# Performance work log

Hardware: AMD Instinct MI355X
Metric: run time of the kernel (lower is better)

## Reference

```python
import jax, jax.numpy as jnp
import numpy as np

B, N, D, H = 4, 1024, 256, 8  # batch, seq, in_dim(=per-head qkv_dim), n_heads


def setup_inputs() -> dict:
    key = jax.random.key(0)
    k1, k2, k3 = jax.random.split(key, 3)
    x = jax.random.normal(k1, (B, N, D), dtype=jnp.float32)
    Wqkv = jax.random.normal(k2, (D, 3 * D * H), dtype=jnp.float32) * 0.02
    bqkv = jnp.zeros((3 * D * H,), dtype=jnp.float32)
    W0 = jax.random.normal(k3, (D * H, D), dtype=jnp.float32) * 0.02
    b0 = jnp.zeros((D,), dtype=jnp.float32)
    return {"x": x, "Wqkv": Wqkv, "bqkv": bqkv, "W0": W0, "b0": b0}


def reference(x, Wqkv, bqkv, W0, b0):
    b, n, d = x.shape
    h = Wqkv.shape[1] // (3 * d)
    qkv = x @ Wqkv + bqkv                      # [b, n, 3*d*h]
    # Faithful to torch: raw row-major reinterpretation of the buffer.
    q, k, v = jnp.reshape(qkv, (3, b, n, d, h))
    score = jnp.einsum('bnqh,btqh->bnth', q, k) * (d ** -0.5)  # [b, n, n, h]
    attn = jax.nn.softmax(score, axis=1)       # softmax over query axis (dim=1), as in source
    # einsum 'bnnh,bnqh->bnqh' = diagonal of attn times v (faithful to source)
    av = jnp.einsum('bnnh,bnqh->bnqh', attn, v)  # [b, n, d, h]
    out = av.reshape(b, n, d * h) @ W0 + b0    # [b, n, d]
    return out
```

## Files before the change

kernel.cpp:

```cpp
#include <hip/hip_runtime.h>


#define SEGSZ 8388608

typedef short v8s __attribute__((ext_vector_type(8)));
typedef float v4f __attribute__((ext_vector_type(4)));

__device__ __forceinline__ ushort f2bf(float v) {
  union { float f; unsigned u; } x; x.f = v;
  const unsigned r = x.u + 0x7fff + ((x.u >> 16) & 1);
  return (ushort)(r >> 16);
}
__device__ __forceinline__ float bf2f(ushort v) {
  union { unsigned u; float f; } x; x.u = ((unsigned)v) << 16;
  return x.f;
}

#define GLOAD_LDS16(g, l)                                            \
  __builtin_amdgcn_global_load_lds(                                  \
      (const __attribute__((address_space(1))) void*)(g),            \
      (__attribute__((address_space(3))) void*)(l), 16, 0, 0)

__global__ __launch_bounds__(256) void prep(
    const float* __restrict__ X, const float* __restrict__ Wqkv,
    const float* __restrict__ W0, ushort* __restrict__ xb,
    ushort* __restrict__ whT, ushort* __restrict__ w0T) {
  __shared__ float T[64][65];
  const int tid = threadIdx.x;
  int bid = blockIdx.x;

  if (bid < 1024) {
    const size_t i = ((size_t)bid * 256 + tid) * 4;
    const float4 v = *(const float4*)&X[i];
    ushort4 hv = {f2bf(v.x), f2bf(v.y), f2bf(v.z), f2bf(v.w)};
    *(ushort4*)&xb[i] = hv;
    return;
  }
  bid -= 1024;
  if (bid < 384) {
    const int n0 = (bid % 96) * 64;
    const int k0 = (bid / 96) * 64;
    {
      const int row = tid >> 2;
      const int c0 = (tid & 3) * 16;
#pragma unroll
      for (int j = 0; j < 16; j += 4) {
        const float4 v = *(const float4*)&Wqkv[(size_t)(k0 + row) * 6144 + n0 + c0 + j];
        T[row][c0 + j + 0] = v.x; T[row][c0 + j + 1] = v.y;
        T[row][c0 + j + 2] = v.z; T[row][c0 + j + 3] = v.w;
      }
    }
    __syncthreads();
    {
      const int nn = tid >> 2;
      const int kk0 = (tid & 3) * 16;
      const int n = n0 + nn;
      const int seg = n >> 11, h = n & 7, d = (n & 2047) >> 3;
      const int p = seg * 2048 + h * 256 + d;
      ushort hv[16];
#pragma unroll
      for (int j = 0; j < 16; ++j) hv[j] = f2bf(T[kk0 + j][nn]);
      const size_t base = (size_t)p * 256 + k0 + kk0;
#pragma unroll
      for (int j = 0; j < 16; j += 8) *(v8s*)&whT[base + j] = *(v8s*)&hv[j];
    }
    return;
  }
  bid -= 384;
  {
    const int e0 = (bid & 3) * 64;
    const int k0 = (bid >> 2) * 64;
    {
      const int row = tid >> 2;
      const int c0 = (tid & 3) * 16;
#pragma unroll
      for (int j = 0; j < 16; j += 4) {
        const float4 v = *(const float4*)&W0[(size_t)(k0 + row) * 256 + e0 + c0 + j];
        T[row][c0 + j + 0] = v.x; T[row][c0 + j + 1] = v.y;
        T[row][c0 + j + 2] = v.z; T[row][c0 + j + 3] = v.w;
      }
    }
    __syncthreads();
    {
      const int ee = tid >> 2;
      const int kk0 = (tid & 3) * 16;
#pragma unroll
      for (int j = 0; j < 16; ++j) {
        const int k = k0 + kk0 + j;
        const int d = k >> 3, h = k & 7;
        w0T[(size_t)(e0 + ee) * 2048 + h * 256 + d] = f2bf(T[kk0 + j][ee]);
      }
    }
  }
}

__global__ __launch_bounds__(256) void qkv_mfma(
    const ushort* __restrict__ xb, const ushort* __restrict__ whT,
    const float* __restrict__ bias, ushort* __restrict__ qkvb) {
  __shared__ ushort As[128 * 32];
  __shared__ ushort Bh[128 * 32];
  const int tid = threadIdx.x;
  const int wave = tid >> 6, lane = tid & 63;
  const int quad = lane >> 4, l15 = lane & 15;
  const int c0 = blockIdx.x * 128;
  const int r0 = blockIdx.y * 128;
  const int wr = (wave >> 1) * 64;
  const int wc = (wave & 1) * 64;

  v4f acc[4][4] = {};

  for (int d0 = 0; d0 < 256; d0 += 32) {
#pragma unroll
    for (int half = 0; half < 2; ++half) {
      const int rr = wave * 32 + half * 16;
      const int row = rr + (lane >> 2);
      const int gcol = d0 + (lane & 3) * 8;
      GLOAD_LDS16(xb + (size_t)(r0 + row) * 256 + gcol, &As[rr * 32]);
      GLOAD_LDS16(whT + (size_t)(c0 + row) * 256 + gcol, &Bh[rr * 32]);
    }
    __syncthreads();

    v8s aF[4], bF[4];
#pragma unroll
    for (int i = 0; i < 4; ++i) {
      aF[i] = *(const v8s*)&As[(wr + i * 16 + l15) * 32 + quad * 8];
      bF[i] = *(const v8s*)&Bh[(wc + i * 16 + l15) * 32 + quad * 8];
    }
#pragma unroll
    for (int ri = 0; ri < 4; ++ri)
#pragma unroll
      for (int ci = 0; ci < 4; ++ci)
        acc[ri][ci] = __builtin_amdgcn_mfma_f32_16x16x32_bf16(
            aF[ri], bF[ci], acc[ri][ci], 0, 0, 0);
    __syncthreads();
  }

#pragma unroll
  for (int ci = 0; ci < 4; ++ci) {
    const int c = c0 + wc + ci * 16 + l15;
    const int cseg = c >> 11;
    const int h = (c & 2047) >> 8;
    const int d = c & 255;
    const float bv = bias[cseg * 2048 + d * 8 + h];
#pragma unroll
    for (int ri = 0; ri < 4; ++ri)
#pragma unroll
      for (int rg = 0; rg < 4; ++rg) {
        const int r = r0 + wr + ri * 16 + quad * 4 + rg;
        const int g = r * 3 + cseg;
        const int seg = g >> 12;
        const int tok = g & 4095;
        float val = acc[ri][ci][rg] + bv;
        if (seg == 0) val *= 0.0625f;
        qkvb[(size_t)seg * SEGSZ + (size_t)tok * 2048 + h * 256 + d] = f2bf(val);
      }
  }
}

__global__ __launch_bounds__(256) void scores_mfma(
    const ushort* __restrict__ qkvb, float* __restrict__ pl,
    float* __restrict__ sd_ws) {
  __shared__ ushort Qs[128 * 32];
  __shared__ ushort Ks[128 * 32];
  __shared__ float redL[2][2][64];

  const int tid = threadIdx.x;
  const int wave = tid >> 6, lane = tid & 63;
  const int quad = lane >> 4, l15 = lane & 15;
  const int bh = blockIdx.z * 8 + blockIdx.x;
  const int tile = blockIdx.y;
  const int tt0 = (tile >> 3) * 128;
  const int nn0 = (tile & 7) * 128;
  const int b = bh >> 3, h = bh & 7;
  const ushort* Qg = qkvb + (size_t)b * 1024 * 2048 + h * 256;
  const ushort* Kg = Qg + SEGSZ;

  const int wr = (wave >> 1) * 64;
  const int wc = (wave & 1) * 64;

  v4f acc[4][4] = {};

  for (int d0 = 0; d0 < 256; d0 += 32) {
#pragma unroll
    for (int half = 0; half < 2; ++half) {
      const int rr = wave * 32 + half * 16;
      const int row = rr + (lane >> 2);
      const int gcol = d0 + (lane & 3) * 8;
      GLOAD_LDS16(Qg + (size_t)(nn0 + row) * 2048 + gcol, &Qs[rr * 32]);
      GLOAD_LDS16(Kg + (size_t)(tt0 + row) * 2048 + gcol, &Ks[rr * 32]);
    }
    __syncthreads();

    v8s aF[4], bF[4];
#pragma unroll
    for (int i = 0; i < 4; ++i) {
      aF[i] = *(const v8s*)&Qs[(wr + i * 16 + l15) * 32 + quad * 8];
      bF[i] = *(const v8s*)&Ks[(wc + i * 16 + l15) * 32 + quad * 8];
    }
#pragma unroll
    for (int ri = 0; ri < 4; ++ri)
#pragma unroll
      for (int ci = 0; ci < 4; ++ci)
        acc[ri][ci] =
            __builtin_amdgcn_mfma_f32_16x16x32_bf16(aF[ri], bF[ci], acc[ri][ci], 0, 0, 0);
    __syncthreads();
  }

  float lsum[4];
#pragma unroll
  for (int ci = 0; ci < 4; ++ci) {
    float s = 0.f;
#pragma unroll
    for (int ri = 0; ri < 4; ++ri)
#pragma unroll
      for (int rg = 0; rg < 4; ++rg) s += __expf(acc[ri][ci][rg]);
    s += __shfl_xor(s, 16, 64);
    s += __shfl_xor(s, 32, 64);
    lsum[ci] = s;
  }
  if (quad == 0) {
#pragma unroll
    for (int ci = 0; ci < 4; ++ci)
      redL[wave & 1][wave >> 1][ci * 16 + l15] = lsum[ci];
  }
  __syncthreads();
  if ((wave >> 1) == 0 && quad == 0) {
#pragma unroll
    for (int ci = 0; ci < 4; ++ci) {
      const int t = tt0 + (wave & 1) * 64 + ci * 16 + l15;
      const float l = lsum[ci] + redL[wave & 1][1][ci * 16 + l15];
      pl[((size_t)bh * 1024 + t) * 8 + (tile & 7)] = l;
    }
  }

  if (tt0 == nn0 && (wave == 0 || wave == 3) && quad == (l15 >> 2)) {
#pragma unroll
    for (int ri = 0; ri < 4; ++ri) {
      const int t = tt0 + (wave & 1) * 64 + ri * 16 + l15;
      sd_ws[(size_t)bh * 1024 + t] = acc[ri][ri][l15 & 3];
    }
  }
}

template <bool ATOMIC>
__global__ __launch_bounds__(256) void av_mfma(
    const ushort* __restrict__ vb, const ushort* __restrict__ w0T,
    const float* __restrict__ pl, const float* __restrict__ sd,
    ushort* __restrict__ partial, float* __restrict__ out) {
  __shared__ ushort As[128 * 32];
  __shared__ ushort Bs[128 * 32];
  __shared__ float diagS[128];
  const int tid = threadIdx.x;
  const int wave = tid >> 6, lane = tid & 63;
  const int quad = lane >> 4, l15 = lane & 15;
  const int e0 = blockIdx.x * 128;
  const int tok0 = blockIdx.y * 128;
  const int h = blockIdx.z;
  const int kbase = h * 256;
  const int wr = (wave >> 1) * 64;
  const int wc = (wave & 1) * 64;

  if (tid < 128) {
    const int bh = (tok0 >> 10) * 8 + h;
    const int t = (tok0 & 1023) + tid;
    const size_t base = ((size_t)bh * 1024 + t) * 8;
    float l = 0.f;
#pragma unroll
    for (int c = 0; c < 8; ++c) l += pl[base + c];
    diagS[tid] = __expf(sd[(size_t)bh * 1024 + t]) / l;
  }

  v4f acc[4][4] = {};

  for (int d0 = 0; d0 < 256; d0 += 32) {
#pragma unroll
    for (int half = 0; half < 2; ++half) {
      const int rr = wave * 32 + half * 16;
      const int row = rr + (lane >> 2);
      const int gcol = kbase + d0 + (lane & 3) * 8;
      GLOAD_LDS16(vb + (size_t)(tok0 + row) * 2048 + gcol, &As[rr * 32]);
      GLOAD_LDS16(w0T + (size_t)(e0 + row) * 2048 + gcol, &Bs[rr * 32]);
    }
    __syncthreads();

    v8s aF[4], bF[4];
#pragma unroll
    for (int i = 0; i < 4; ++i) {
      aF[i] = *(const v8s*)&As[(wr + i * 16 + l15) * 32 + quad * 8];
      bF[i] = *(const v8s*)&Bs[(wc + i * 16 + l15) * 32 + quad * 8];
    }
#pragma unroll
    for (int ri = 0; ri < 4; ++ri)
#pragma unroll
      for (int ci = 0; ci < 4; ++ci)
        acc[ri][ci] =
            __builtin_amdgcn_mfma_f32_16x16x32_bf16(aF[ri], bF[ci], acc[ri][ci], 0, 0, 0);
    __syncthreads();
  }

#pragma unroll
  for (int ri = 0; ri < 4; ++ri)
#pragma unroll
    for (int rg = 0; rg < 4; ++rg) {
      const int lrow = wr + ri * 16 + quad * 4 + rg;
      const int tok = tok0 + lrow;
      const float dg = diagS[lrow];
#pragma unroll
      for (int ci = 0; ci < 4; ++ci) {
        const int e = e0 + wc + ci * 16 + l15;
        const float val = acc[ri][ci][rg] * dg;
        if (ATOMIC)
          atomicAdd(&out[(size_t)tok * 256 + e], val);
        else
          partial[(size_t)h * 1048576 + (size_t)tok * 256 + e] = f2bf(val);
      }
    }
}

__global__ void init_out(const float* __restrict__ b0, float* __restrict__ out) {
  const int i = blockIdx.x * 256 + threadIdx.x;
  const int e0 = (i & 63) << 2;
  *(float4*)&out[(size_t)i * 4] = *(const float4*)&b0[e0];
}

__global__ void reduce_out(const ushort* __restrict__ partial,
                           const float* __restrict__ b0, float* __restrict__ out) {
  const int i = blockIdx.x * 256 + threadIdx.x;
  const int e0 = (i & 63) << 2;
  float4 a = *(const float4*)&b0[e0];
#pragma unroll
  for (int h = 0; h < 8; ++h) {
    const ushort4 p = *(const ushort4*)&partial[(size_t)h * 1048576 + (size_t)i * 4];
    a.x += bf2f(p.x); a.y += bf2f(p.y); a.z += bf2f(p.z); a.w += bf2f(p.w);
  }
  *(float4*)&out[(size_t)i * 4] = a;
}

extern "C" void kernel_launch(void* const* d_in, const int* in_sizes, int n_in,
                              void* d_out, int out_size, void* d_ws, size_t ws_size,
                              hipStream_t stream) {
  const float* x    = (const float*)d_in[0];
  const float* Wqkv = (const float*)d_in[1];
  const float* bqkv = (const float*)d_in[2];
  const float* W0   = (const float*)d_in[3];
  const float* b0   = (const float*)d_in[4];
  float* out = (float*)d_out;

  float*  pl   = (float*)d_ws;
  float*  sd   = pl + 262144;
  ushort* qkvb = (ushort*)(sd + 32768);
  ushort* xb   = qkvb + 3 * (size_t)SEGSZ;
  ushort* whT  = xb + 1048576;
  ushort* w0T  = whT + 1572864;
  ushort* partial = w0T + 524288;

  ushort* vb = qkvb + 2 * (size_t)SEGSZ;

  const size_t need_base =
      (size_t)(262144 + 32768) * 4 + (size_t)SEGSZ * 3 * 2 +
      (size_t)(1048576 + 1572864 + 524288) * 2;
  const bool full = ws_size >= need_base + (size_t)8 * 1048576 * 2;

  prep<<<1536, 256, 0, stream>>>(x, Wqkv, W0, xb, whT, w0T);
  qkv_mfma<<<dim3(48, 32), 256, 0, stream>>>(xb, whT, bqkv, qkvb);
  scores_mfma<<<dim3(8, 64, 4), 256, 0, stream>>>(qkvb, pl, sd);
  if (full) {
    av_mfma<false><<<dim3(2, 32, 8), 256, 0, stream>>>(vb, w0T, pl, sd, partial, out);
    reduce_out<<<1024, 256, 0, stream>>>(partial, b0, out);
  } else {
    init_out<<<1024, 256, 0, stream>>>(b0, out);
    av_mfma<true><<<dim3(2, 32, 8), 256, 0, stream>>>(vb, w0T, pl, sd, nullptr, out);
  }
}
```

Baseline: 141.4 us.

## Keep K strip resident in LDS for scores and widen QKV/AV block tiles

The scores kernel now loads a full 128x256 K strip into LDS once per block and loops over four 128-row Q tiles, accumulating column exp-sums across them. That cuts K reloads and the partial-sum array from 8 slots to 2 per token. The QKV and AV GEMMs move to 512-thread blocks with 256-wide tiles (256 rows in QKV, the full 256 output columns in AV), so shared operands are reused more and the grid is halved. In exchange, the scores kernel uses about 72KB of LDS, runs 4x fewer blocks, and has a long serial loop, which lowers occupancy and parallelism.

```diff
diff --git a/kernel.cpp b/kernel.cpp
--- a/kernel.cpp
+++ b/kernel.cpp
@@ -94,16 +94,16 @@
   }
 }
 
-__global__ __launch_bounds__(256) void qkv_mfma(
+__global__ __launch_bounds__(512) void qkv_mfma(
     const ushort* __restrict__ xb, const ushort* __restrict__ whT,
     const float* __restrict__ bias, ushort* __restrict__ qkvb) {
-  __shared__ ushort As[128 * 32];
+  __shared__ ushort As[256 * 32];
   __shared__ ushort Bh[128 * 32];
   const int tid = threadIdx.x;
   const int wave = tid >> 6, lane = tid & 63;
   const int quad = lane >> 4, l15 = lane & 15;
   const int c0 = blockIdx.x * 128;
-  const int r0 = blockIdx.y * 128;
+  const int r0 = blockIdx.y * 256;
   const int wr = (wave >> 1) * 64;
   const int wc = (wave & 1) * 64;
 
@@ -111,12 +111,15 @@
 
   for (int d0 = 0; d0 < 256; d0 += 32) {
 #pragma unroll
-    for (int half = 0; half < 2; ++half) {
-      const int rr = wave * 32 + half * 16;
-      const int row = rr + (lane >> 2);
-      const int gcol = d0 + (lane & 3) * 8;
-      GLOAD_LDS16(xb + (size_t)(r0 + row) * 256 + gcol, &As[rr * 32]);
-      GLOAD_LDS16(whT + (size_t)(c0 + row) * 256 + gcol, &Bh[rr * 32]);
+    for (int h2 = 0; h2 < 2; ++h2) {
+      const int rr = wave * 32 + h2 * 16;
+      const int row = rr + (lane >> 2);
+      GLOAD_LDS16(xb + (size_t)(r0 + row) * 256 + d0 + (lane & 3) * 8, &As[rr * 32]);
+    }
+    {
+      const int rr = wave * 16;
+      const int row = rr + (lane >> 2);
+      GLOAD_LDS16(whT + (size_t)(c0 + row) * 256 + d0 + (lane & 3) * 8, &Bh[rr * 32]);
     }
     __syncthreads();
 
@@ -160,17 +163,17 @@
 __global__ __launch_bounds__(256) void scores_mfma(
     const ushort* __restrict__ qkvb, float* __restrict__ pl,
     float* __restrict__ sd_ws) {
+  __shared__ ushort Ks[8 * 128 * 32];
   __shared__ ushort Qs[128 * 32];
-  __shared__ ushort Ks[128 * 32];
   __shared__ float redL[2][2][64];
 
   const int tid = threadIdx.x;
   const int wave = tid >> 6, lane = tid & 63;
   const int quad = lane >> 4, l15 = lane & 15;
   const int bh = blockIdx.z * 8 + blockIdx.x;
-  const int tile = blockIdx.y;
-  const int tt0 = (tile >> 3) * 128;
-  const int nn0 = (tile & 7) * 128;
+  const int strip = blockIdx.y;
+  const int tt0 = (strip >> 1) * 128;
+  const int half = strip & 1;
   const int b = bh >> 3, h = bh & 7;
   const ushort* Qg = qkvb + (size_t)b * 1024 * 2048 + h * 256;
   const ushort* Kg = Qg + SEGSZ;
@@ -178,108 +181,124 @@
   const int wr = (wave >> 1) * 64;
   const int wc = (wave & 1) * 64;
 
-  v4f acc[4][4] = {};
-
-  for (int d0 = 0; d0 < 256; d0 += 32) {
-#pragma unroll
-    for (int half = 0; half < 2; ++half) {
-      const int rr = wave * 32 + half * 16;
-      const int row = rr + (lane >> 2);
-      const int gcol = d0 + (lane & 3) * 8;
-      GLOAD_LDS16(Qg + (size_t)(nn0 + row) * 2048 + gcol, &Qs[rr * 32]);
-      GLOAD_LDS16(Kg + (size_t)(tt0 + row) * 2048 + gcol, &Ks[rr * 32]);
-    }
-    __syncthreads();
-
-    v8s aF[4], bF[4];
-#pragma unroll
-    for (int i = 0; i < 4; ++i) {
-      aF[i] = *(const v8s*)&Qs[(wr + i * 16 + l15) * 32 + quad * 8];
-      bF[i] = *(const v8s*)&Ks[(wc + i * 16 + l15) * 32 + quad * 8];
-    }
-#pragma unroll
-    for (int ri = 0; ri < 4; ++ri)
-#pragma unroll
-      for (int ci = 0; ci < 4; ++ci)
-        acc[ri][ci] =
-            __builtin_amdgcn_mfma_f32_16x16x32_bf16(aF[ri], bF[ci], acc[ri][ci], 0, 0, 0);
-    __syncthreads();
-  }
-
-  float lsum[4];
+#pragma unroll
+  for (int c = 0; c < 8; ++c)
+#pragma unroll
+    for (int h2 = 0; h2 < 2; ++h2) {
+      const int rr = wave * 32 + h2 * 16;
+      const int row = rr + (lane >> 2);
+      GLOAD_LDS16(Kg + (size_t)(tt0 + row) * 2048 + c * 32 + (lane & 3) * 8,
+                  &Ks[c * 4096 + rr * 32]);
+    }
+
+  float colsum[4] = {0.f, 0.f, 0.f, 0.f};
+
+  for (int i = 0; i < 4; ++i) {
+    const int nn0 = half * 512 + i * 128;
+    v4f acc[4][4] = {};
+#pragma unroll
+    for (int c = 0; c < 8; ++c) {
+#pragma unroll
+      for (int h2 = 0; h2 < 2; ++h2) {
+        const int rr = wave * 32 + h2 * 16;
+        const int row = rr + (lane >> 2);
+        GLOAD_LDS16(Qg + (size_t)(nn0 + row) * 2048 + c * 32 + (lane & 3) * 8,
+                    &Qs[rr * 32]);
+      }
+      __syncthreads();
+
+      v8s aF[4], bF[4];
+#pragma unroll
+      for (int j = 0; j < 4; ++j) {
+        aF[j] = *(const v8s*)&Qs[(wr + j * 16 + l15) * 32 + quad * 8];
+        bF[j] = *(const v8s*)&Ks[c * 4096 + (wc + j * 16 + l15) * 32 + quad * 8];
+      }
+#pragma unroll
+      for (int ri = 0; ri < 4; ++ri)
+#pragma unroll
+        for (int ci = 0; ci < 4; ++ci)
+          acc[ri][ci] = __builtin_amdgcn_mfma_f32_16x16x32_bf16(
+              aF[ri], bF[ci], acc[ri][ci], 0, 0, 0);
+      __syncthreads();
+    }
+#pragma unroll
+    for (int ci = 0; ci < 4; ++ci) {
+      float s = 0.f;
+#pragma unroll
+      for (int ri = 0; ri < 4; ++ri)
+#pragma unroll
+        for (int rg = 0; rg < 4; ++rg) s += __expf(acc[ri][ci][rg]);
+      colsum[ci] += s;
+    }
+    if (nn0 == tt0 && (wave == 0 || wave == 3) && quad == (l15 >> 2)) {
+#pragma unroll
+      for (int ri = 0; ri < 4; ++ri) {
+        const int t = tt0 + (wave & 1) * 64 + ri * 16 + l15;
+        sd_ws[(size_t)bh * 1024 + t] = acc[ri][ri][l15 & 3];
+      }
+    }
+  }
+
 #pragma unroll
   for (int ci = 0; ci < 4; ++ci) {
-    float s = 0.f;
-#pragma unroll
-    for (int ri = 0; ri < 4; ++ri)
-#pragma unroll
-      for (int rg = 0; rg < 4; ++rg) s += __expf(acc[ri][ci][rg]);
-    s += __shfl_xor(s, 16, 64);
-    s += __shfl_xor(s, 32, 64);
-    lsum[ci] = s;
+    colsum[ci] += __shfl_xor(colsum[ci], 16, 64);
+    colsum[ci] += __shfl_xor(colsum[ci], 32, 64);
   }
   if (quad == 0) {
 #pragma unroll
     for (int ci = 0; ci < 4; ++ci)
-      redL[wave & 1][wave >> 1][ci * 16 + l15] = lsum[ci];
+      redL[wave & 1][wave >> 1][ci * 16 + l15] = colsum[ci];
   }
   __syncthreads();
   if ((wave >> 1) == 0 && quad == 0) {
 #pragma unroll
     for (int ci = 0; ci < 4; ++ci) {
       const int t = tt0 + (wave & 1) * 64 + ci * 16 + l15;
-      const float l = lsum[ci] + redL[wave & 1][1][ci * 16 + l15];
-      pl[((size_t)bh * 1024 + t) * 8 + (tile & 7)] = l;
-    }
-  }
-
-  if (tt0 == nn0 && (wave == 0 || wave == 3) && quad == (l15 >> 2)) {
-#pragma unroll
-    for (int ri = 0; ri < 4; ++ri) {
-      const int t = tt0 + (wave & 1) * 64 + ri * 16 + l15;
-      sd_ws[(size_t)bh * 1024 + t] = acc[ri][ri][l15 & 3];
+      const float l = colsum[ci] + redL[wave & 1][1][ci * 16 + l15];
+      pl[((size_t)bh * 1024 + t) * 2 + half] = l;
     }
   }
 }
 
 template <bool ATOMIC>
-__global__ __launch_bounds__(256) void av_mfma(
+__global__ __launch_bounds__(512) void av_mfma(
     const ushort* __restrict__ vb, const ushort* __restrict__ w0T,
     const float* __restrict__ pl, const float* __restrict__ sd,
     ushort* __restrict__ partial, float* __restrict__ out) {
   __shared__ ushort As[128 * 32];
-  __shared__ ushort Bs[128 * 32];
+  __shared__ ushort Bs[256 * 32];
   __shared__ float diagS[128];
   const int tid = threadIdx.x;
   const int wave = tid >> 6, lane = tid & 63;
   const int quad = lane >> 4, l15 = lane & 15;
-  const int e0 = blockIdx.x * 128;
-  const int tok0 = blockIdx.y * 128;
-  const int h = blockIdx.z;
+  const int tok0 = blockIdx.x * 128;
+  const int h = blockIdx.y;
   const int kbase = h * 256;
-  const int wr = (wave >> 1) * 64;
-  const int wc = (wave & 1) * 64;
+  const int wr = (wave >> 2) * 64;
+  const int wc = (wave & 3) * 64;
 
   if (tid < 128) {
     const int bh = (tok0 >> 10) * 8 + h;
     const int t = (tok0 & 1023) + tid;
-    const size_t base = ((size_t)bh * 1024 + t) * 8;
-    float l = 0.f;
-#pragma unroll
-    for (int c = 0; c < 8; ++c) l += pl[base + c];
-    diagS[tid] = __expf(sd[(size_t)bh * 1024 + t]) / l;
+    const size_t base = ((size_t)bh * 1024 + t) * 2;
+    diagS[tid] = __expf(sd[(size_t)bh * 1024 + t]) / (pl[base] + pl[base + 1]);
   }
 
   v4f acc[4][4] = {};
 
   for (int d0 = 0; d0 < 256; d0 += 32) {
-#pragma unroll
-    for (int half = 0; half < 2; ++half) {
-      const int rr = wave * 32 + half * 16;
-      const int row = rr + (lane >> 2);
-      const int gcol = kbase + d0 + (lane & 3) * 8;
-      GLOAD_LDS16(vb + (size_t)(tok0 + row) * 2048 + gcol, &As[rr * 32]);
-      GLOAD_LDS16(w0T + (size_t)(e0 + row) * 2048 + gcol, &Bs[rr * 32]);
+    {
+      const int rr = wave * 16;
+      const int row = rr + (lane >> 2);
+      GLOAD_LDS16(vb + (size_t)(tok0 + row) * 2048 + kbase + d0 + (lane & 3) * 8,
+                  &As[rr * 32]);
+    }
+#pragma unroll
+    for (int h2 = 0; h2 < 2; ++h2) {
+      const int rr = wave * 32 + h2 * 16;
+      const int row = rr + (lane >> 2);
+      GLOAD_LDS16(w0T + (size_t)row * 2048 + kbase + d0 + (lane & 3) * 8,
+                  &Bs[rr * 32]);
     }
     __syncthreads();
 
@@ -307,7 +326,7 @@
       const float dg = diagS[lrow];
 #pragma unroll
       for (int ci = 0; ci < 4; ++ci) {
-        const int e = e0 + wc + ci * 16 + l15;
+        const int e = wc + ci * 16 + l15;
         const float val = acc[ri][ci][rg] * dg;
         if (ATOMIC)
           atomicAdd(&out[(size_t)tok * 256 + e], val);
@@ -347,7 +366,7 @@
   float* out = (float*)d_out;
 
   float*  pl   = (float*)d_ws;
-  float*  sd   = pl + 262144;
+  float*  sd   = pl + 65536;
   ushort* qkvb = (ushort*)(sd + 32768);
   ushort* xb   = qkvb + 3 * (size_t)SEGSZ;
   ushort* whT  = xb + 1048576;
@@ -357,18 +376,18 @@
   ushort* vb = qkvb + 2 * (size_t)SEGSZ;
 
   const size_t need_base =
-      (size_t)(262144 + 32768) * 4 + (size_t)SEGSZ * 3 * 2 +
+      (size_t)(65536 + 32768) * 4 + (size_t)SEGSZ * 3 * 2 +
       (size_t)(1048576 + 1572864 + 524288) * 2;
   const bool full = ws_size >= need_base + (size_t)8 * 1048576 * 2;
 
   prep<<<1536, 256, 0, stream>>>(x, Wqkv, W0, xb, whT, w0T);
-  qkv_mfma<<<dim3(48, 32), 256, 0, stream>>>(xb, whT, bqkv, qkvb);
-  scores_mfma<<<dim3(8, 64, 4), 256, 0, stream>>>(qkvb, pl, sd);
+  qkv_mfma<<<dim3(48, 16), 512, 0, stream>>>(xb, whT, bqkv, qkvb);
+  scores_mfma<<<dim3(8, 16, 4), 256, 0, stream>>>(qkvb, pl, sd);
   if (full) {
-    av_mfma<false><<<dim3(2, 32, 8), 256, 0, stream>>>(vb, w0T, pl, sd, partial, out);
+    av_mfma<false><<<dim3(32, 8), 512, 0, stream>>>(vb, w0T, pl, sd, partial, out);
     reduce_out<<<1024, 256, 0, stream>>>(partial, b0, out);
   } else {
     init_out<<<1024, 256, 0, stream>>>(b0, out);
-    av_mfma<true><<<dim3(2, 32, 8), 256, 0, stream>>>(vb, w0T, pl, sd, nullptr, out);
-  }
-}
+    av_mfma<true><<<dim3(32, 8), 512, 0, stream>>>(vb, w0T, pl, sd, nullptr, out);
+  }
+}
```

New measurement: 142.4 us. Within noise of the previous version (+0.8%).
